# Kernel tuning notes

Measured on AMD Instinct MI355X. Metric: run time of the kernel, lower is better.

Reference implementation:

```python
import jax, jax.numpy as jnp
import numpy as np

H = 16  # num_attention_heads


def setup_inputs() -> dict:
    key = jax.random.key(0)
    ks = jax.random.split(key, 4)
    B, S, D = 2, 2048, 1024
    hidden_states = jax.random.normal(ks[0], (B, S, D), dtype=jnp.float32)
    attention_mask = jnp.zeros((B, 1, 1, S), dtype=jnp.float32)
    scale = 1.0 / np.sqrt(D)
    Wq = jax.random.normal(ks[1], (D, D), dtype=jnp.float32) * scale
    Wk = jax.random.normal(ks[2], (D, D), dtype=jnp.float32) * scale
    Wv = jax.random.normal(ks[3], (D, D), dtype=jnp.float32) * scale
    bq = jnp.zeros((D,), dtype=jnp.float32)
    bk = jnp.zeros((D,), dtype=jnp.float32)
    bv = jnp.zeros((D,), dtype=jnp.float32)
    return {"hidden_states": hidden_states, "attention_mask": attention_mask,
            "Wq": Wq, "bq": bq, "Wk": Wk, "bk": bk, "Wv": Wv, "bv": bv}


def reference(hidden_states, attention_mask, Wq, bq, Wk, bk, Wv, bv):
    B, S, D = hidden_states.shape
    Dh = D // H

    def proj(W, b):
        # torch Linear: x @ W.T + b ; reshape to [B, H, S, Dh]
        y = jnp.einsum('bsd,ed->bse', hidden_states, W) + b
        return y.reshape(B, S, H, Dh).transpose(0, 2, 1, 3)

    q = proj(Wq, bq)
    k = proj(Wk, bk)
    v = proj(Wv, bv)

    scores = jnp.einsum('bhqd,bhkd->bhqk', q, k) / jnp.sqrt(jnp.float32(Dh))
    scores = scores + attention_mask  # additive mask broadcast [B,1,1,S]
    probs = jax.nn.softmax(scores, axis=-1)  # [B,H,Sq,Sk]
    out_attention_scores = probs.sum(axis=-2).sum(axis=-2)  # [B, Sk]
    # dropout prob = 0 (eval) -> identity
    context = jnp.einsum('bhqk,bhkd->bhqd', probs, v)
    context = context.transpose(0, 2, 1, 3).reshape(B, S, D)
    return context, out_attention_scores
```

## Files before the change

### kernel.cpp

```cpp
#include <hip/hip_runtime.h>
#include <hip/hip_bf16.h>
#include <stdint.h>

typedef unsigned short u16;
typedef __attribute__((ext_vector_type(8))) unsigned short u16x8;
typedef __attribute__((ext_vector_type(4))) unsigned short u16x4;
typedef __attribute__((ext_vector_type(8))) __bf16 bf16x8;
typedef __attribute__((ext_vector_type(4))) float f32x4;

#define LOG2E 1.44269504088896340736f

#if defined(__has_builtin)
#if __has_builtin(__builtin_amdgcn_exp2f)
#define EXP2(x) __builtin_amdgcn_exp2f(x)
#endif
#endif
#ifndef EXP2
#define EXP2(x) exp2f(x)
#endif

__device__ __forceinline__ f32x4 mfma16(u16x8 a, u16x8 b, f32x4 c) {
  return __builtin_amdgcn_mfma_f32_16x16x32_bf16(
      __builtin_bit_cast(bf16x8, a), __builtin_bit_cast(bf16x8, b), c, 0, 0, 0);
}

__device__ __forceinline__ u16 f2bf(float f) {
  unsigned u = __builtin_bit_cast(unsigned, f);
  return (u16)((u + 0x7fffu + ((u >> 16) & 1u)) >> 16);
}

__device__ __forceinline__ unsigned cvtpk(float a, float b) {
  unsigned r;
  asm volatile("v_cvt_pk_bf16_f32 %0, %1, %2" : "=v"(r) : "v"(a), "v"(b));
  return r;
}

__device__ __forceinline__ void gload_lds16(const void* g, void* l) {
  __builtin_amdgcn_global_load_lds(
      (__attribute__((address_space(1))) void*)const_cast<void*>(g),
      (__attribute__((address_space(3))) void*)l, 16, 0, 0);
}

#define SWZ(row, colbyte) ((((row) * 128) + (colbyte)) ^ (((row) & 7) << 4))

__global__ void cast_f32_bf16(const float* __restrict__ src, u16* __restrict__ dst, int n4) {
  int i = blockIdx.x * blockDim.x + threadIdx.x;
  if (i < n4) {
    f32x4 v = ((const f32x4*)src)[i];
    u16x4 o;
    o[0] = f2bf(v[0]); o[1] = f2bf(v[1]); o[2] = f2bf(v[2]); o[3] = f2bf(v[3]);
    ((u16x4*)dst)[i] = o;
  }
}

__global__ __launch_bounds__(256) void gemm_qkv(
    const u16* __restrict__ A, const u16* __restrict__ Bm,
    const float* __restrict__ bq, const float* __restrict__ bk, const float* __restrict__ bv,
    u16* __restrict__ Qb, u16* __restrict__ Kb, u16* __restrict__ VTb) {
  __shared__ __align__(16) u16 Asm[128 * 32];
  __shared__ __align__(16) u16 Bsm[128 * 32];
  const int tid = threadIdx.x;
  const int wave = tid >> 6, lane = tid & 63;
  const int lq = lane & 15, lg = lane >> 4;
  const int wr = wave >> 1, wc = wave & 1;
  const int m0 = blockIdx.y * 128, n0 = blockIdx.x * 128;

  f32x4 zero = {0.f, 0.f, 0.f, 0.f};
  f32x4 acc[4][4];
#pragma unroll
  for (int mi = 0; mi < 4; ++mi)
#pragma unroll
    for (int ni = 0; ni < 4; ++ni) acc[mi][ni] = zero;

  for (int kt = 0; kt < 32; ++kt) {
    const int k0 = kt * 32;
    __syncthreads();
#pragma unroll
    for (int c = 0; c < 2; ++c) {
      const int idx = wave * 2 + c;
      const u16* ga = A + (size_t)(m0 + idx * 16 + (lane >> 2)) * 1024 + k0 + (lane & 3) * 8;
      gload_lds16(ga, (char*)Asm + idx * 1024);
      const u16* gb = Bm + (size_t)(n0 + idx * 16 + (lane >> 2)) * 1024 + k0 + (lane & 3) * 8;
      gload_lds16(gb, (char*)Bsm + idx * 1024);
    }
    __syncthreads();

    u16x8 af[4], bfr[4];
#pragma unroll
    for (int mi = 0; mi < 4; ++mi)
      af[mi] = *(const u16x8*)&Asm[(wr * 64 + mi * 16 + lq) * 32 + lg * 8];
#pragma unroll
    for (int ni = 0; ni < 4; ++ni)
      bfr[ni] = *(const u16x8*)&Bsm[(wc * 64 + ni * 16 + lq) * 32 + lg * 8];
#pragma unroll
    for (int mi = 0; mi < 4; ++mi)
#pragma unroll
      for (int ni = 0; ni < 4; ++ni)
        acc[mi][ni] = mfma16(af[mi], bfr[ni], acc[mi][ni]);
  }

  const int which = n0 >> 10;
  const float* bias = (which == 0) ? bq : ((which == 1) ? bk : bv);
  const float scl = (which == 0) ? (0.125f * LOG2E) : 1.0f;
#pragma unroll
  for (int mi = 0; mi < 4; ++mi) {
    const int m = m0 + wr * 64 + mi * 16 + lg * 4;
    const int bb = m >> 11;
    const int s = m & 2047;
#pragma unroll
    for (int ni = 0; ni < 4; ++ni) {
      const int n = n0 + wc * 64 + ni * 16 + lq;
      const int d = n & 1023;
      const int h = d >> 6, dh = d & 63;
      const float bi = bias[d];
#pragma unroll
      for (int r = 0; r < 4; ++r) {
        float v = (acc[mi][ni][r] + bi) * scl;
        if (which == 2)
          VTb[(((size_t)bb * 16 + h) * 64 + dh) * 2048 + (size_t)(s + r)] = f2bf(v);
        else {
          u16* dst = (which == 0) ? Qb : Kb;
          dst[(((size_t)bb * 16 + h) * 2048 + (size_t)(s + r)) * 64 + dh] = f2bf(v);
        }
      }
    }
  }
}

__global__ __launch_bounds__(512) void attn_fused(
    const u16* __restrict__ Qb, const u16* __restrict__ Kb, const u16* __restrict__ VTb,
    const float* __restrict__ maskg, float* __restrict__ out_ctx, float* __restrict__ winv) {
  __shared__ __align__(16) u16 Kl[2][4096];
  __shared__ __align__(16) u16 VTl[2][4096];
  __shared__ __align__(16) u16 Pl[8][2048];

  const int tid = threadIdx.x;
  const int w = tid >> 6, lane = tid & 63;
  const int lq = lane & 15, lg = lane >> 4;
  const int bid = (blockIdx.x & 7) * 32 + (blockIdx.x >> 3);
  const int qt = bid & 7, bh = bid >> 3;
  const int b = bh >> 4, h = bh & 15;
  const int qw = qt * 256 + w * 32;

  const u16* qp0 = Qb + ((size_t)bh * 2048 + qw + lq) * 64 + lg * 8;
  const u16* qp1 = qp0 + 16 * 64;
  const u16x8 qa00 = *(const u16x8*)qp0, qa01 = *(const u16x8*)(qp0 + 32);
  const u16x8 qa10 = *(const u16x8*)qp1, qa11 = *(const u16x8*)(qp1 + 32);

  const char* Kbase = (const char*)(Kb + (size_t)bh * 2048 * 64);
  const char* VTbase = (const char*)(VTb + (size_t)bh * 64 * 2048);
  const float* mbase = maskg + b * 2048;

  const int srow = tid >> 3;
  const int scol = ((tid & 7) * 16) ^ ((srow & 7) << 4);
  char* kb0 = (char*)&Kl[0][0] + w * 1024;
  char* kb1 = (char*)&Kl[1][0] + w * 1024;
  char* vb0 = (char*)&VTl[0][0] + w * 1024;
  char* vb1 = (char*)&VTl[1][0] + w * 1024;

  auto stageK = [&](int kt, int buf) {
    gload_lds16(Kbase + (size_t)(kt * 64 + srow) * 128 + scol, buf ? kb1 : kb0);
  };
  auto stageVT = [&](int kt, int buf) {
    gload_lds16(VTbase + (size_t)srow * 4096 + (size_t)kt * 128 + scol, buf ? vb1 : vb0);
  };

  f32x4 acc[2][4];
  {
    f32x4 zero = {0.f, 0.f, 0.f, 0.f};
#pragma unroll
    for (int g = 0; g < 2; ++g)
#pragma unroll
      for (int ni = 0; ni < 4; ++ni) acc[g][ni] = zero;
  }
  float l_lo = 0.f, l_hi = 0.f;
  char* Pw = (char*)&Pl[w][0];

  stageK(0, 0);
  stageVT(0, 0);
  __syncthreads();
  for (int kt = 0; kt < 32; ++kt) {
    const int cur = kt & 1;
    if (kt + 1 < 32) { stageK(kt + 1, cur ^ 1); stageVT(kt + 1, cur ^ 1); }
    const char* Kt = (const char*)&Kl[cur][0];
    const char* Vt = (const char*)&VTl[cur][0];

#pragma unroll
    for (int chunk = 0; chunk < 4; ++chunk) {
      const int krow = chunk * 16 + lq;
      const u16x8 ka0 = *(const u16x8*)(Kt + SWZ(krow, lg * 16));
      const u16x8 ka1 = *(const u16x8*)(Kt + SWZ(krow, 64 + lg * 16));
      f32x4 z = {0.f, 0.f, 0.f, 0.f};
      f32x4 slo = mfma16(ka0, qa00, z);
      slo = mfma16(ka1, qa01, slo);
      f32x4 shi = mfma16(ka0, qa10, z);
      shi = mfma16(ka1, qa11, shi);
      const f32x4 mv = *(const f32x4*)(mbase + kt * 64 + chunk * 16 + lg * 4);
      const float m0 = mv[0] * LOG2E, m1 = mv[1] * LOG2E;
      const float m2 = mv[2] * LOG2E, m3 = mv[3] * LOG2E;
      const float pl0 = EXP2(slo[0] + m0), pl1 = EXP2(slo[1] + m1);
      const float pl2 = EXP2(slo[2] + m2), pl3 = EXP2(slo[3] + m3);
      const float ph0 = EXP2(shi[0] + m0), ph1 = EXP2(shi[1] + m1);
      const float ph2 = EXP2(shi[2] + m2), ph3 = EXP2(shi[3] + m3);
      l_lo += (pl0 + pl1) + (pl2 + pl3);
      l_hi += (ph0 + ph1) + (ph2 + ph3);
      uint2 wlo, whi;
      wlo.x = cvtpk(pl0, pl1); wlo.y = cvtpk(pl2, pl3);
      whi.x = cvtpk(ph0, ph1); whi.y = cvtpk(ph2, ph3);
      *(uint2*)(Pw + SWZ(lq, chunk * 32 + lg * 8)) = wlo;
      *(uint2*)(Pw + SWZ(16 + lq, chunk * 32 + lg * 8)) = whi;
    }

#pragma unroll
    for (int kc = 0; kc < 2; ++kc) {
      const u16x8 pa0 = *(const u16x8*)(Pw + SWZ(lq, kc * 64 + lg * 16));
      const u16x8 pa1 = *(const u16x8*)(Pw + SWZ(16 + lq, kc * 64 + lg * 16));
#pragma unroll
      for (int ni = 0; ni < 4; ++ni) {
        const u16x8 vb = *(const u16x8*)(Vt + SWZ(ni * 16 + lq, kc * 64 + lg * 16));
        acc[0][ni] = mfma16(pa0, vb, acc[0][ni]);
        acc[1][ni] = mfma16(pa1, vb, acc[1][ni]);
      }
    }
    __syncthreads();
  }

  l_lo += __shfl_xor(l_lo, 16); l_lo += __shfl_xor(l_lo, 32);
  l_hi += __shfl_xor(l_hi, 16); l_hi += __shfl_xor(l_hi, 32);
  const float il_lo = 1.0f / l_lo;
  const float il_hi = 1.0f / l_hi;
  if (lg == 0) {
    winv[bh * 2048 + qw + lq] = il_lo;
    winv[bh * 2048 + qw + 16 + lq] = il_hi;
  }
  f32x4 il4[2];
#pragma unroll
  for (int r = 0; r < 4; ++r) {
    il4[0][r] = __shfl(il_lo, lg * 4 + r);
    il4[1][r] = __shfl(il_hi, lg * 4 + r);
  }
#pragma unroll
  for (int g = 0; g < 2; ++g) {
    const int qrow = b * 2048 + qw + g * 16 + lg * 4;
#pragma unroll
    for (int ni = 0; ni < 4; ++ni) {
      const int dh = h * 64 + ni * 16 + lq;
#pragma unroll
      for (int r = 0; r < 4; ++r)
        out_ctx[(size_t)(qrow + r) * 1024 + dh] = acc[g][ni][r] * il4[g][r];
    }
  }
}

__global__ __launch_bounds__(512) void colsum_kernel(
    const u16* __restrict__ Qb, const u16* __restrict__ Kb,
    const float* __restrict__ maskg, const float* __restrict__ winv,
    float* __restrict__ out_cs) {
  __shared__ __align__(16) u16 Ql[2][4096];

  const int tid = threadIdx.x;
  const int w = tid >> 6, lane = tid & 63;
  const int lq = lane & 15, lg = lane >> 4;
  const int bid = (blockIdx.x & 7) * 64 + (blockIdx.x >> 3);
  const int ktile = bid & 15, bh = bid >> 4;
  const int b = bh >> 4;
  const int kbase = ktile * 128 + w * 16;

  const u16* kp = Kb + ((size_t)bh * 2048 + kbase + lq) * 64 + lg * 8;
  const u16x8 kb0 = *(const u16x8*)kp, kb1 = *(const u16x8*)(kp + 32);
  const float mvl = maskg[b * 2048 + kbase + lq] * LOG2E;
  const float* wbase = winv + bh * 2048;
  const char* Qbase = (const char*)(Qb + (size_t)bh * 2048 * 64);

  const int srow = tid >> 3;
  const int scol = ((tid & 7) * 16) ^ ((srow & 7) << 4);
  char* qd0 = (char*)&Ql[0][0] + w * 1024;
  char* qd1 = (char*)&Ql[1][0] + w * 1024;
  auto stageQ = [&](int qt, int buf) {
    gload_lds16(Qbase + (size_t)(qt * 64 + srow) * 128 + scol, buf ? qd1 : qd0);
  };

  float c = 0.f;
  stageQ(0, 0);
  __syncthreads();
  for (int qt = 0; qt < 32; ++qt) {
    const int cur = qt & 1;
    if (qt + 1 < 32) stageQ(qt + 1, cur ^ 1);
    const char* Qt = (const char*)&Ql[cur][0];
#pragma unroll
    for (int chunk = 0; chunk < 4; ++chunk) {
      const u16x8 qf0 = *(const u16x8*)(Qt + SWZ(chunk * 16 + lq, lg * 16));
      const u16x8 qf1 = *(const u16x8*)(Qt + SWZ(chunk * 16 + lq, 64 + lg * 16));
      f32x4 z = {0.f, 0.f, 0.f, 0.f};
      f32x4 s = mfma16(qf0, kb0, z);
      s = mfma16(qf1, kb1, s);
      const f32x4 wv = *(const f32x4*)(wbase + qt * 64 + chunk * 16 + lg * 4);
      c += EXP2(s[0] + mvl) * wv[0] + EXP2(s[1] + mvl) * wv[1] +
           EXP2(s[2] + mvl) * wv[2] + EXP2(s[3] + mvl) * wv[3];
    }
    __syncthreads();
  }
  c += __shfl_xor(c, 16);
  c += __shfl_xor(c, 32);
  if (lg == 0) atomicAdd(&out_cs[b * 2048 + kbase + lq], c);
}

extern "C" void kernel_launch(void* const* d_in, const int* in_sizes, int n_in,
                              void* d_out, int out_size, void* d_ws, size_t ws_size,
                              hipStream_t stream) {
  (void)in_sizes; (void)n_in; (void)out_size; (void)ws_size;
  const float* X    = (const float*)d_in[0];
  const float* mask = (const float*)d_in[1];
  const float* Wq   = (const float*)d_in[2];
  const float* bq   = (const float*)d_in[3];
  const float* Wk   = (const float*)d_in[4];
  const float* bk   = (const float*)d_in[5];
  const float* Wv   = (const float*)d_in[6];
  const float* bv   = (const float*)d_in[7];
  float* out = (float*)d_out;

  char* ws = (char*)d_ws;
  u16* Xb   = (u16*)(ws);
  u16* Wcat = (u16*)(ws + 8388608);
  u16* Qb   = (u16*)(ws + 14680064);
  u16* Kb   = (u16*)(ws + 23068672);
  u16* VTb  = (u16*)(ws + 31457280);
  float* winv = (float*)ws;

  cast_f32_bf16<<<4096, 256, 0, stream>>>(X, Xb, 1048576);
  cast_f32_bf16<<<1024, 256, 0, stream>>>(Wq, Wcat, 262144);
  cast_f32_bf16<<<1024, 256, 0, stream>>>(Wk, Wcat + 1048576, 262144);
  cast_f32_bf16<<<1024, 256, 0, stream>>>(Wv, Wcat + 2097152, 262144);

  hipMemsetAsync(out + 4194304, 0, 4096 * sizeof(float), stream);

  gemm_qkv<<<dim3(24, 32), 256, 0, stream>>>(Xb, Wcat, bq, bk, bv, Qb, Kb, VTb);

  attn_fused<<<256, 512, 0, stream>>>(Qb, Kb, VTb, mask, out, winv);
  colsum_kernel<<<512, 512, 0, stream>>>(Qb, Kb, mask, winv, out + 4194304);
}
```

Before: 156.5 us.

## Fuse column-sum into two-pass attention kernel and merge weight casts

```diff
diff --git a/kernel.cpp b/kernel.cpp
--- a/kernel.cpp
+++ b/kernel.cpp
@@ -14,9 +14,15 @@
 #if __has_builtin(__builtin_amdgcn_exp2f)
 #define EXP2(x) __builtin_amdgcn_exp2f(x)
 #endif
+#if __has_builtin(__builtin_amdgcn_logf)
+#define LOG2F(x) __builtin_amdgcn_logf(x)
+#endif
 #endif
 #ifndef EXP2
 #define EXP2(x) exp2f(x)
+#endif
+#ifndef LOG2F
+#define LOG2F(x) log2f(x)
 #endif
 
 __device__ __forceinline__ f32x4 mfma16(u16x8 a, u16x8 b, f32x4 c) {
@@ -51,6 +57,17 @@
     o[0] = f2bf(v[0]); o[1] = f2bf(v[1]); o[2] = f2bf(v[2]); o[3] = f2bf(v[3]);
     ((u16x4*)dst)[i] = o;
   }
+}
+
+__global__ void cast3_f32_bf16(const float* __restrict__ s0, const float* __restrict__ s1,
+                               const float* __restrict__ s2, u16* __restrict__ dst) {
+  const int seg = blockIdx.x >> 10;
+  const int i = (blockIdx.x & 1023) * blockDim.x + threadIdx.x;
+  const float* src = (seg == 0) ? s0 : ((seg == 1) ? s1 : s2);
+  f32x4 v = ((const f32x4*)src)[i];
+  u16x4 o;
+  o[0] = f2bf(v[0]); o[1] = f2bf(v[1]); o[2] = f2bf(v[2]); o[3] = f2bf(v[3]);
+  ((u16x4*)(dst + (size_t)seg * 1048576))[i] = o;
 }
 
 __global__ __launch_bounds__(256) void gemm_qkv(
@@ -127,20 +144,23 @@
   }
 }
 
-__global__ __launch_bounds__(512) void attn_fused(
+__global__ __launch_bounds__(256) void attn_fused(
     const u16* __restrict__ Qb, const u16* __restrict__ Kb, const u16* __restrict__ VTb,
-    const float* __restrict__ maskg, float* __restrict__ out_ctx, float* __restrict__ winv) {
+    const float* __restrict__ maskg, float* __restrict__ out_ctx, float* __restrict__ out_cs) {
   __shared__ __align__(16) u16 Kl[2][4096];
   __shared__ __align__(16) u16 VTl[2][4096];
-  __shared__ __align__(16) u16 Pl[8][2048];
+  __shared__ __align__(16) u16 Pl[4][2048];
+  __shared__ float cs_lds[2048];
 
   const int tid = threadIdx.x;
   const int w = tid >> 6, lane = tid & 63;
   const int lq = lane & 15, lg = lane >> 4;
-  const int bid = (blockIdx.x & 7) * 32 + (blockIdx.x >> 3);
-  const int qt = bid & 7, bh = bid >> 3;
+  const int bid = (blockIdx.x & 7) * 64 + (blockIdx.x >> 3);
+  const int qt = bid & 15, bh = bid >> 4;
   const int b = bh >> 4, h = bh & 15;
-  const int qw = qt * 256 + w * 32;
+  const int qw = qt * 128 + w * 32;
+
+  for (int i = tid; i < 2048; i += 256) cs_lds[i] = 0.f;
 
   const u16* qp0 = Qb + ((size_t)bh * 2048 + qw + lq) * 64 + lg * 8;
   const u16* qp1 = qp0 + 16 * 64;
@@ -151,40 +171,27 @@
   const char* VTbase = (const char*)(VTb + (size_t)bh * 64 * 2048);
   const float* mbase = maskg + b * 2048;
 
-  const int srow = tid >> 3;
-  const int scol = ((tid & 7) * 16) ^ ((srow & 7) << 4);
-  char* kb0 = (char*)&Kl[0][0] + w * 1024;
-  char* kb1 = (char*)&Kl[1][0] + w * 1024;
-  char* vb0 = (char*)&VTl[0][0] + w * 1024;
-  char* vb1 = (char*)&VTl[1][0] + w * 1024;
+  const int r0 = w * 8 + (lane >> 3);
+  const int s0c = ((lane & 7) * 16) ^ ((r0 & 7) << 4);
 
   auto stageK = [&](int kt, int buf) {
-    gload_lds16(Kbase + (size_t)(kt * 64 + srow) * 128 + scol, buf ? kb1 : kb0);
+    const char* src = Kbase + (size_t)(kt * 64) * 128;
+    gload_lds16(src + (size_t)r0 * 128 + s0c, (char*)&Kl[buf][0] + w * 1024);
+    gload_lds16(src + (size_t)(r0 + 32) * 128 + s0c, (char*)&Kl[buf][0] + 4096 + w * 1024);
   };
   auto stageVT = [&](int kt, int buf) {
-    gload_lds16(VTbase + (size_t)srow * 4096 + (size_t)kt * 128 + scol, buf ? vb1 : vb0);
+    const char* src = VTbase + (size_t)kt * 128;
+    gload_lds16(src + (size_t)r0 * 4096 + s0c, (char*)&VTl[buf][0] + w * 1024);
+    gload_lds16(src + (size_t)(r0 + 32) * 4096 + s0c, (char*)&VTl[buf][0] + 4096 + w * 1024);
   };
 
-  f32x4 acc[2][4];
-  {
-    f32x4 zero = {0.f, 0.f, 0.f, 0.f};
-#pragma unroll
-    for (int g = 0; g < 2; ++g)
-#pragma unroll
-      for (int ni = 0; ni < 4; ++ni) acc[g][ni] = zero;
-  }
   float l_lo = 0.f, l_hi = 0.f;
-  char* Pw = (char*)&Pl[w][0];
-
   stageK(0, 0);
-  stageVT(0, 0);
   __syncthreads();
   for (int kt = 0; kt < 32; ++kt) {
     const int cur = kt & 1;
-    if (kt + 1 < 32) { stageK(kt + 1, cur ^ 1); stageVT(kt + 1, cur ^ 1); }
+    if (kt + 1 < 32) stageK(kt + 1, cur ^ 1);
     const char* Kt = (const char*)&Kl[cur][0];
-    const char* Vt = (const char*)&VTl[cur][0];
-
 #pragma unroll
     for (int chunk = 0; chunk < 4; ++chunk) {
       const int krow = chunk * 16 + lq;
@@ -196,17 +203,70 @@
       f32x4 shi = mfma16(ka0, qa10, z);
       shi = mfma16(ka1, qa11, shi);
       const f32x4 mv = *(const f32x4*)(mbase + kt * 64 + chunk * 16 + lg * 4);
-      const float m0 = mv[0] * LOG2E, m1 = mv[1] * LOG2E;
-      const float m2 = mv[2] * LOG2E, m3 = mv[3] * LOG2E;
-      const float pl0 = EXP2(slo[0] + m0), pl1 = EXP2(slo[1] + m1);
-      const float pl2 = EXP2(slo[2] + m2), pl3 = EXP2(slo[3] + m3);
-      const float ph0 = EXP2(shi[0] + m0), ph1 = EXP2(shi[1] + m1);
-      const float ph2 = EXP2(shi[2] + m2), ph3 = EXP2(shi[3] + m3);
-      l_lo += (pl0 + pl1) + (pl2 + pl3);
-      l_hi += (ph0 + ph1) + (ph2 + ph3);
+#pragma unroll
+      for (int r = 0; r < 4; ++r) {
+        l_lo += EXP2(fmaf(mv[r], LOG2E, slo[r]));
+        l_hi += EXP2(fmaf(mv[r], LOG2E, shi[r]));
+      }
+    }
+    __syncthreads();
+  }
+  l_lo += __shfl_xor(l_lo, 16); l_lo += __shfl_xor(l_lo, 32);
+  l_hi += __shfl_xor(l_hi, 16); l_hi += __shfl_xor(l_hi, 32);
+  const float lw_lo = -LOG2F(l_lo);
+  const float lw_hi = -LOG2F(l_hi);
+
+  f32x4 acc[2][4];
+  {
+    f32x4 zero = {0.f, 0.f, 0.f, 0.f};
+#pragma unroll
+    for (int g = 0; g < 2; ++g)
+#pragma unroll
+      for (int ni = 0; ni < 4; ++ni) acc[g][ni] = zero;
+  }
+  char* Pw = (char*)&Pl[w][0];
+
+  stageK(0, 0);
+  stageVT(0, 0);
+  __syncthreads();
+  for (int kt = 0; kt < 32; ++kt) {
+    const int cur = kt & 1;
+    if (kt + 1 < 32) { stageK(kt + 1, cur ^ 1); stageVT(kt + 1, cur ^ 1); }
+    const char* Kt = (const char*)&Kl[cur][0];
+    const char* Vt = (const char*)&VTl[cur][0];
+
+#pragma unroll
+    for (int chunk = 0; chunk < 4; ++chunk) {
+      const int krow = chunk * 16 + lq;
+      const u16x8 ka0 = *(const u16x8*)(Kt + SWZ(krow, lg * 16));
+      const u16x8 ka1 = *(const u16x8*)(Kt + SWZ(krow, 64 + lg * 16));
+      f32x4 z = {0.f, 0.f, 0.f, 0.f};
+      f32x4 slo = mfma16(ka0, qa00, z);
+      slo = mfma16(ka1, qa01, slo);
+      f32x4 shi = mfma16(ka0, qa10, z);
+      shi = mfma16(ka1, qa11, shi);
+      const f32x4 mv = *(const f32x4*)(mbase + kt * 64 + chunk * 16 + lg * 4);
+      float pl[4], ph[4];
+      f32x4 c;
+#pragma unroll
+      for (int r = 0; r < 4; ++r) {
+        pl[r] = EXP2(fmaf(mv[r], LOG2E, slo[r] + lw_lo));
+        ph[r] = EXP2(fmaf(mv[r], LOG2E, shi[r] + lw_hi));
+        c[r] = pl[r] + ph[r];
+      }
+#pragma unroll
+      for (int msk = 1; msk <= 8; msk <<= 1) {
+#pragma unroll
+        for (int r = 0; r < 4; ++r) c[r] += __shfl_xor(c[r], msk);
+      }
+      if (lq == 0) {
+        const int kb = kt * 64 + chunk * 16 + lg * 4;
+#pragma unroll
+        for (int r = 0; r < 4; ++r) atomicAdd(&cs_lds[kb + r], c[r]);
+      }
       uint2 wlo, whi;
-      wlo.x = cvtpk(pl0, pl1); wlo.y = cvtpk(pl2, pl3);
-      whi.x = cvtpk(ph0, ph1); whi.y = cvtpk(ph2, ph3);
+      wlo.x = cvtpk(pl[0], pl[1]); wlo.y = cvtpk(pl[2], pl[3]);
+      whi.x = cvtpk(ph[0], ph[1]); whi.y = cvtpk(ph[2], ph[3]);
       *(uint2*)(Pw + SWZ(lq, chunk * 32 + lg * 8)) = wlo;
       *(uint2*)(Pw + SWZ(16 + lq, chunk * 32 + lg * 8)) = whi;
     }
@@ -225,20 +285,6 @@
     __syncthreads();
   }
 
-  l_lo += __shfl_xor(l_lo, 16); l_lo += __shfl_xor(l_lo, 32);
-  l_hi += __shfl_xor(l_hi, 16); l_hi += __shfl_xor(l_hi, 32);
-  const float il_lo = 1.0f / l_lo;
-  const float il_hi = 1.0f / l_hi;
-  if (lg == 0) {
-    winv[bh * 2048 + qw + lq] = il_lo;
-    winv[bh * 2048 + qw + 16 + lq] = il_hi;
-  }
-  f32x4 il4[2];
-#pragma unroll
-  for (int r = 0; r < 4; ++r) {
-    il4[0][r] = __shfl(il_lo, lg * 4 + r);
-    il4[1][r] = __shfl(il_hi, lg * 4 + r);
-  }
 #pragma unroll
   for (int g = 0; g < 2; ++g) {
     const int qrow = b * 2048 + qw + g * 16 + lg * 4;
@@ -247,62 +293,13 @@
       const int dh = h * 64 + ni * 16 + lq;
 #pragma unroll
       for (int r = 0; r < 4; ++r)
-        out_ctx[(size_t)(qrow + r) * 1024 + dh] = acc[g][ni][r] * il4[g][r];
-    }
-  }
-}
-
-__global__ __launch_bounds__(512) void colsum_kernel(
-    const u16* __restrict__ Qb, const u16* __restrict__ Kb,
-    const float* __restrict__ maskg, const float* __restrict__ winv,
-    float* __restrict__ out_cs) {
-  __shared__ __align__(16) u16 Ql[2][4096];
-
-  const int tid = threadIdx.x;
-  const int w = tid >> 6, lane = tid & 63;
-  const int lq = lane & 15, lg = lane >> 4;
-  const int bid = (blockIdx.x & 7) * 64 + (blockIdx.x >> 3);
-  const int ktile = bid & 15, bh = bid >> 4;
-  const int b = bh >> 4;
-  const int kbase = ktile * 128 + w * 16;
-
-  const u16* kp = Kb + ((size_t)bh * 2048 + kbase + lq) * 64 + lg * 8;
-  const u16x8 kb0 = *(const u16x8*)kp, kb1 = *(const u16x8*)(kp + 32);
-  const float mvl = maskg[b * 2048 + kbase + lq] * LOG2E;
-  const float* wbase = winv + bh * 2048;
-  const char* Qbase = (const char*)(Qb + (size_t)bh * 2048 * 64);
-
-  const int srow = tid >> 3;
-  const int scol = ((tid & 7) * 16) ^ ((srow & 7) << 4);
-  char* qd0 = (char*)&Ql[0][0] + w * 1024;
-  char* qd1 = (char*)&Ql[1][0] + w * 1024;
-  auto stageQ = [&](int qt, int buf) {
-    gload_lds16(Qbase + (size_t)(qt * 64 + srow) * 128 + scol, buf ? qd1 : qd0);
-  };
-
-  float c = 0.f;
-  stageQ(0, 0);
+        out_ctx[(size_t)(qrow + r) * 1024 + dh] = acc[g][ni][r];
+    }
+  }
+
   __syncthreads();
-  for (int qt = 0; qt < 32; ++qt) {
-    const int cur = qt & 1;
-    if (qt + 1 < 32) stageQ(qt + 1, cur ^ 1);
-    const char* Qt = (const char*)&Ql[cur][0];
-#pragma unroll
-    for (int chunk = 0; chunk < 4; ++chunk) {
-      const u16x8 qf0 = *(const u16x8*)(Qt + SWZ(chunk * 16 + lq, lg * 16));
-      const u16x8 qf1 = *(const u16x8*)(Qt + SWZ(chunk * 16 + lq, 64 + lg * 16));
-      f32x4 z = {0.f, 0.f, 0.f, 0.f};
-      f32x4 s = mfma16(qf0, kb0, z);
-      s = mfma16(qf1, kb1, s);
-      const f32x4 wv = *(const f32x4*)(wbase + qt * 64 + chunk * 16 + lg * 4);
-      c += EXP2(s[0] + mvl) * wv[0] + EXP2(s[1] + mvl) * wv[1] +
-           EXP2(s[2] + mvl) * wv[2] + EXP2(s[3] + mvl) * wv[3];
-    }
-    __syncthreads();
-  }
-  c += __shfl_xor(c, 16);
-  c += __shfl_xor(c, 32);
-  if (lg == 0) atomicAdd(&out_cs[b * 2048 + kbase + lq], c);
+  for (int i = tid; i < 2048; i += 256)
+    atomicAdd(&out_cs[b * 2048 + i], cs_lds[i]);
 }
 
 extern "C" void kernel_launch(void* const* d_in, const int* in_sizes, int n_in,
@@ -325,17 +322,13 @@
   u16* Qb   = (u16*)(ws + 14680064);
   u16* Kb   = (u16*)(ws + 23068672);
   u16* VTb  = (u16*)(ws + 31457280);
-  float* winv = (float*)ws;
 
   cast_f32_bf16<<<4096, 256, 0, stream>>>(X, Xb, 1048576);
-  cast_f32_bf16<<<1024, 256, 0, stream>>>(Wq, Wcat, 262144);
-  cast_f32_bf16<<<1024, 256, 0, stream>>>(Wk, Wcat + 1048576, 262144);
-  cast_f32_bf16<<<1024, 256, 0, stream>>>(Wv, Wcat + 2097152, 262144);
+  cast3_f32_bf16<<<3072, 256, 0, stream>>>(Wq, Wk, Wv, Wcat);
 
   hipMemsetAsync(out + 4194304, 0, 4096 * sizeof(float), stream);
 
   gemm_qkv<<<dim3(24, 32), 256, 0, stream>>>(Xb, Wcat, bq, bk, bv, Qb, Kb, VTb);
 
-  attn_fused<<<256, 512, 0, stream>>>(Qb, Kb, VTb, mask, out, winv);
-  colsum_kernel<<<512, 512, 0, stream>>>(Qb, Kb, mask, winv, out + 4194304);
-}
+  attn_fused<<<512, 256, 0, stream>>>(Qb, Kb, VTb, mask, out, out + 4194304);
+}
```

New measurement: 200.1 us. 27.8% more time.

## Halve per-block query tile in attention and colsum to double grid size

Applied to the files above, without the earlier changes.

```diff
diff --git a/kernel.cpp b/kernel.cpp
--- a/kernel.cpp
+++ b/kernel.cpp
@@ -51,6 +51,17 @@
     o[0] = f2bf(v[0]); o[1] = f2bf(v[1]); o[2] = f2bf(v[2]); o[3] = f2bf(v[3]);
     ((u16x4*)dst)[i] = o;
   }
+}
+
+__global__ void cast3_f32_bf16(const float* __restrict__ s0, const float* __restrict__ s1,
+                               const float* __restrict__ s2, u16* __restrict__ dst) {
+  const int seg = blockIdx.x >> 10;
+  const int i = (blockIdx.x & 1023) * blockDim.x + threadIdx.x;
+  const float* src = (seg == 0) ? s0 : ((seg == 1) ? s1 : s2);
+  f32x4 v = ((const f32x4*)src)[i];
+  u16x4 o;
+  o[0] = f2bf(v[0]); o[1] = f2bf(v[1]); o[2] = f2bf(v[2]); o[3] = f2bf(v[3]);
+  ((u16x4*)(dst + (size_t)seg * 1048576))[i] = o;
 }
 
 __global__ __launch_bounds__(256) void gemm_qkv(
@@ -127,25 +138,24 @@
   }
 }
 
-__global__ __launch_bounds__(512) void attn_fused(
+__global__ __launch_bounds__(512) void attn_main(
     const u16* __restrict__ Qb, const u16* __restrict__ Kb, const u16* __restrict__ VTb,
     const float* __restrict__ maskg, float* __restrict__ out_ctx, float* __restrict__ winv) {
   __shared__ __align__(16) u16 Kl[2][4096];
   __shared__ __align__(16) u16 VTl[2][4096];
-  __shared__ __align__(16) u16 Pl[8][2048];
+  __shared__ __align__(16) u16 Pl[8][1024];
 
   const int tid = threadIdx.x;
   const int w = tid >> 6, lane = tid & 63;
   const int lq = lane & 15, lg = lane >> 4;
-  const int bid = (blockIdx.x & 7) * 32 + (blockIdx.x >> 3);
-  const int qt = bid & 7, bh = bid >> 3;
+  const int bid = (blockIdx.x & 7) * 64 + (blockIdx.x >> 3);
+  const int qt = bid & 15, bh = bid >> 4;
   const int b = bh >> 4, h = bh & 15;
-  const int qw = qt * 256 + w * 32;
-
-  const u16* qp0 = Qb + ((size_t)bh * 2048 + qw + lq) * 64 + lg * 8;
-  const u16* qp1 = qp0 + 16 * 64;
-  const u16x8 qa00 = *(const u16x8*)qp0, qa01 = *(const u16x8*)(qp0 + 32);
-  const u16x8 qa10 = *(const u16x8*)qp1, qa11 = *(const u16x8*)(qp1 + 32);
+  const int qw = qt * 128 + w * 16;
+
+  const u16* qp = Qb + ((size_t)bh * 2048 + qw + lq) * 64 + lg * 8;
+  const u16x8 qa0 = *(const u16x8*)qp;
+  const u16x8 qa1 = *(const u16x8*)(qp + 32);
 
   const char* Kbase = (const char*)(Kb + (size_t)bh * 2048 * 64);
   const char* VTbase = (const char*)(VTb + (size_t)bh * 64 * 2048);
@@ -153,27 +163,25 @@
 
   const int srow = tid >> 3;
   const int scol = ((tid & 7) * 16) ^ ((srow & 7) << 4);
-  char* kb0 = (char*)&Kl[0][0] + w * 1024;
-  char* kb1 = (char*)&Kl[1][0] + w * 1024;
-  char* vb0 = (char*)&VTl[0][0] + w * 1024;
-  char* vb1 = (char*)&VTl[1][0] + w * 1024;
+  char* kd0 = (char*)&Kl[0][0] + w * 1024;
+  char* kd1 = (char*)&Kl[1][0] + w * 1024;
+  char* vd0 = (char*)&VTl[0][0] + w * 1024;
+  char* vd1 = (char*)&VTl[1][0] + w * 1024;
 
   auto stageK = [&](int kt, int buf) {
-    gload_lds16(Kbase + (size_t)(kt * 64 + srow) * 128 + scol, buf ? kb1 : kb0);
+    gload_lds16(Kbase + (size_t)(kt * 64 + srow) * 128 + scol, buf ? kd1 : kd0);
   };
   auto stageVT = [&](int kt, int buf) {
-    gload_lds16(VTbase + (size_t)srow * 4096 + (size_t)kt * 128 + scol, buf ? vb1 : vb0);
+    gload_lds16(VTbase + (size_t)srow * 4096 + (size_t)kt * 128 + scol, buf ? vd1 : vd0);
   };
 
-  f32x4 acc[2][4];
+  f32x4 acc[4];
   {
     f32x4 zero = {0.f, 0.f, 0.f, 0.f};
 #pragma unroll
-    for (int g = 0; g < 2; ++g)
-#pragma unroll
-      for (int ni = 0; ni < 4; ++ni) acc[g][ni] = zero;
-  }
-  float l_lo = 0.f, l_hi = 0.f;
+    for (int ni = 0; ni < 4; ++ni) acc[ni] = zero;
+  }
+  float l_l = 0.f;
   char* Pw = (char*)&Pl[w][0];
 
   stageK(0, 0);
@@ -191,68 +199,52 @@
       const u16x8 ka0 = *(const u16x8*)(Kt + SWZ(krow, lg * 16));
       const u16x8 ka1 = *(const u16x8*)(Kt + SWZ(krow, 64 + lg * 16));
       f32x4 z = {0.f, 0.f, 0.f, 0.f};
-      f32x4 slo = mfma16(ka0, qa00, z);
-      slo = mfma16(ka1, qa01, slo);
-      f32x4 shi = mfma16(ka0, qa10, z);
-      shi = mfma16(ka1, qa11, shi);
+      f32x4 s = mfma16(ka0, qa0, z);
+      s = mfma16(ka1, qa1, s);
       const f32x4 mv = *(const f32x4*)(mbase + kt * 64 + chunk * 16 + lg * 4);
-      const float m0 = mv[0] * LOG2E, m1 = mv[1] * LOG2E;
-      const float m2 = mv[2] * LOG2E, m3 = mv[3] * LOG2E;
-      const float pl0 = EXP2(slo[0] + m0), pl1 = EXP2(slo[1] + m1);
-      const float pl2 = EXP2(slo[2] + m2), pl3 = EXP2(slo[3] + m3);
-      const float ph0 = EXP2(shi[0] + m0), ph1 = EXP2(shi[1] + m1);
-      const float ph2 = EXP2(shi[2] + m2), ph3 = EXP2(shi[3] + m3);
-      l_lo += (pl0 + pl1) + (pl2 + pl3);
-      l_hi += (ph0 + ph1) + (ph2 + ph3);
-      uint2 wlo, whi;
-      wlo.x = cvtpk(pl0, pl1); wlo.y = cvtpk(pl2, pl3);
-      whi.x = cvtpk(ph0, ph1); whi.y = cvtpk(ph2, ph3);
-      *(uint2*)(Pw + SWZ(lq, chunk * 32 + lg * 8)) = wlo;
-      *(uint2*)(Pw + SWZ(16 + lq, chunk * 32 + lg * 8)) = whi;
+      float p[4];
+#pragma unroll
+      for (int r = 0; r < 4; ++r) {
+        p[r] = EXP2(fmaf(mv[r], LOG2E, s[r]));
+        l_l += p[r];
+      }
+      uint2 wp;
+      wp.x = cvtpk(p[0], p[1]); wp.y = cvtpk(p[2], p[3]);
+      *(uint2*)(Pw + SWZ(lq, chunk * 32 + lg * 8)) = wp;
     }
 
 #pragma unroll
     for (int kc = 0; kc < 2; ++kc) {
-      const u16x8 pa0 = *(const u16x8*)(Pw + SWZ(lq, kc * 64 + lg * 16));
-      const u16x8 pa1 = *(const u16x8*)(Pw + SWZ(16 + lq, kc * 64 + lg * 16));
+      const u16x8 pa = *(const u16x8*)(Pw + SWZ(lq, kc * 64 + lg * 16));
 #pragma unroll
       for (int ni = 0; ni < 4; ++ni) {
         const u16x8 vb = *(const u16x8*)(Vt + SWZ(ni * 16 + lq, kc * 64 + lg * 16));
-        acc[0][ni] = mfma16(pa0, vb, acc[0][ni]);
-        acc[1][ni] = mfma16(pa1, vb, acc[1][ni]);
+        acc[ni] = mfma16(pa, vb, acc[ni]);
       }
     }
     __syncthreads();
   }
 
-  l_lo += __shfl_xor(l_lo, 16); l_lo += __shfl_xor(l_lo, 32);
-  l_hi += __shfl_xor(l_hi, 16); l_hi += __shfl_xor(l_hi, 32);
-  const float il_lo = 1.0f / l_lo;
-  const float il_hi = 1.0f / l_hi;
-  if (lg == 0) {
-    winv[bh * 2048 + qw + lq] = il_lo;
-    winv[bh * 2048 + qw + 16 + lq] = il_hi;
-  }
-  f32x4 il4[2];
-#pragma unroll
-  for (int r = 0; r < 4; ++r) {
-    il4[0][r] = __shfl(il_lo, lg * 4 + r);
-    il4[1][r] = __shfl(il_hi, lg * 4 + r);
-  }
-#pragma unroll
-  for (int g = 0; g < 2; ++g) {
-    const int qrow = b * 2048 + qw + g * 16 + lg * 4;
-#pragma unroll
-    for (int ni = 0; ni < 4; ++ni) {
-      const int dh = h * 64 + ni * 16 + lq;
-#pragma unroll
-      for (int r = 0; r < 4; ++r)
-        out_ctx[(size_t)(qrow + r) * 1024 + dh] = acc[g][ni][r] * il4[g][r];
-    }
-  }
-}
-
-__global__ __launch_bounds__(512) void colsum_kernel(
+  l_l += __shfl_xor(l_l, 16);
+  l_l += __shfl_xor(l_l, 32);
+  const float il = 1.0f / l_l;
+  if (lg == 0) winv[bh * 2048 + qw + lq] = il;
+
+  f32x4 il4;
+#pragma unroll
+  for (int r = 0; r < 4; ++r) il4[r] = __shfl(il, lg * 4 + r);
+
+  const int qrow = b * 2048 + qw + lg * 4;
+#pragma unroll
+  for (int ni = 0; ni < 4; ++ni) {
+    const int dh = h * 64 + ni * 16 + lq;
+#pragma unroll
+    for (int r = 0; r < 4; ++r)
+      out_ctx[(size_t)(qrow + r) * 1024 + dh] = acc[ni][r] * il4[r];
+  }
+}
+
+__global__ __launch_bounds__(256) void colsum_kernel(
     const u16* __restrict__ Qb, const u16* __restrict__ Kb,
     const float* __restrict__ maskg, const float* __restrict__ winv,
     float* __restrict__ out_cs) {
@@ -261,10 +253,10 @@
   const int tid = threadIdx.x;
   const int w = tid >> 6, lane = tid & 63;
   const int lq = lane & 15, lg = lane >> 4;
-  const int bid = (blockIdx.x & 7) * 64 + (blockIdx.x >> 3);
-  const int ktile = bid & 15, bh = bid >> 4;
+  const int bid = (blockIdx.x & 7) * 128 + (blockIdx.x >> 3);
+  const int ktile = bid & 31, bh = bid >> 5;
   const int b = bh >> 4;
-  const int kbase = ktile * 128 + w * 16;
+  const int kbase = ktile * 64 + w * 16;
 
   const u16* kp = Kb + ((size_t)bh * 2048 + kbase + lq) * 64 + lg * 8;
   const u16x8 kb0 = *(const u16x8*)kp, kb1 = *(const u16x8*)(kp + 32);
@@ -272,12 +264,15 @@
   const float* wbase = winv + bh * 2048;
   const char* Qbase = (const char*)(Qb + (size_t)bh * 2048 * 64);
 
-  const int srow = tid >> 3;
-  const int scol = ((tid & 7) * 16) ^ ((srow & 7) << 4);
+  const int r0 = tid >> 3;
+  const int scol = ((tid & 7) * 16) ^ ((r0 & 7) << 4);
   char* qd0 = (char*)&Ql[0][0] + w * 1024;
   char* qd1 = (char*)&Ql[1][0] + w * 1024;
   auto stageQ = [&](int qt, int buf) {
-    gload_lds16(Qbase + (size_t)(qt * 64 + srow) * 128 + scol, buf ? qd1 : qd0);
+    const char* src = Qbase + (size_t)(qt * 64) * 128;
+    char* d = buf ? qd1 : qd0;
+    gload_lds16(src + (size_t)r0 * 128 + scol, d);
+    gload_lds16(src + (size_t)(r0 + 32) * 128 + scol, d + 4096);
   };
 
   float c = 0.f;
@@ -325,17 +320,15 @@
   u16* Qb   = (u16*)(ws + 14680064);
   u16* Kb   = (u16*)(ws + 23068672);
   u16* VTb  = (u16*)(ws + 31457280);
-  float* winv = (float*)ws;
+  float* winv = (float*)(ws + 39845888);
 
   cast_f32_bf16<<<4096, 256, 0, stream>>>(X, Xb, 1048576);
-  cast_f32_bf16<<<1024, 256, 0, stream>>>(Wq, Wcat, 262144);
-  cast_f32_bf16<<<1024, 256, 0, stream>>>(Wk, Wcat + 1048576, 262144);
-  cast_f32_bf16<<<1024, 256, 0, stream>>>(Wv, Wcat + 2097152, 262144);
+  cast3_f32_bf16<<<3072, 256, 0, stream>>>(Wq, Wk, Wv, Wcat);
 
   hipMemsetAsync(out + 4194304, 0, 4096 * sizeof(float), stream);
 
   gemm_qkv<<<dim3(24, 32), 256, 0, stream>>>(Xb, Wcat, bq, bk, bv, Qb, Kb, VTb);
 
-  attn_fused<<<256, 512, 0, stream>>>(Qb, Kb, VTb, mask, out, winv);
-  colsum_kernel<<<512, 512, 0, stream>>>(Qb, Kb, mask, winv, out + 4194304);
-}
+  attn_main<<<512, 512, 0, stream>>>(Qb, Kb, VTb, mask, out, winv);
+  colsum_kernel<<<1024, 256, 0, stream>>>(Qb, Kb, mask, winv, out + 4194304);
+}
```

New measurement: 158.8 us. No clear change (+1.5%).
